# Performance work log

Measured on AMD Instinct MI355X. Metric: run time of the kernel, lower is better.

The kernel has to match this reference:

```python
import jax, jax.numpy as jnp
import numpy as np
from jax import lax

NB, C, HEADS, DH, MULT = 3, 64, 4, 16, 4  # num_blocks, dim, heads, dim_head, ffn mult

def _dw(x, k):
    # depthwise conv, NHWC, kernel HWIO with I=1, O=C, SAME padding
    return lax.conv_general_dilated(x, k, (1, 1), 'SAME',
                                    dimension_numbers=('NHWC', 'HWIO', 'NHWC'),
                                    feature_group_count=x.shape[-1])

def _l2n(t, eps=1e-6):
    # torch F.normalize(p=2, eps): x / max(||x||, eps) over last dim
    n = jnp.sqrt(jnp.sum(t * t, -1, keepdims=True))
    return t / jnp.maximum(n, eps)

def _ln(x, g, b, eps=1e-5):
    mu = jnp.mean(x, -1, keepdims=True)
    var = jnp.mean((x - mu) ** 2, -1, keepdims=True)
    return (x - mu) / jnp.sqrt(var + eps) * g + b

def _msa(x, m, Wq, Wk, Wv, resc, Wp, bp, pe1, pe2, w1, b1, w2, b2, dwk, db):
    # x, m: [b,h,w,c] (NHWC)
    b, h, w, c = x.shape
    n = h * w
    xf = x.reshape(b, n, c)
    q = xf @ Wq
    k = xf @ Wk
    v = xf @ Wv
    # mask-guided mechanism (1x1 convs == channel matmuls, 5x5 depthwise)
    m1 = m @ w1 + b1
    am = jax.nn.sigmoid(_dw(m1 @ w2 + b2, dwk) + db)
    ma = (m1 * am + m1).reshape(b, n, c)
    vg = v * ma  # mask gating of V (elementwise, head split commutes)
    hd = lambda t: t.reshape(b, n, HEADS, DH).transpose(0, 2, 3, 1)  # b,H,d,n
    qh = _l2n(hd(q))
    kh = _l2n(hd(k))
    vh = hd(vg)
    # transposed (channel) attention: [d,n]x[n,d] -> [d,d]
    attn = jnp.einsum('bhdn,bhen->bhde', kh, qh) * resc[None, :, None, None]
    attn = jax.nn.softmax(attn, -1)
    o = jnp.einsum('bhde,bhen->bhdn', attn, vh).transpose(0, 3, 1, 2).reshape(b, n, c)
    out_c = (o @ Wp + bp).reshape(b, h, w, c)
    # positional embedding on ungated v_inp: dwconv3 -> GELU -> dwconv3
    vi = v.reshape(b, h, w, c)
    out_p = _dw(jax.nn.gelu(_dw(vi, pe1), approximate=False), pe2)
    return out_c + out_p

def _ff(x, w1, dwk, w2):
    h1 = jax.nn.gelu(x @ w1, approximate=False)          # 1x1 conv expand
    h2 = jax.nn.gelu(_dw(h1, dwk), approximate=False)     # 3x3 depthwise
    return h2 @ w2                                        # 1x1 conv project

def setup_inputs() -> dict:
    key = jax.random.key(0)
    ks = iter(jax.random.split(key, 24))
    r = lambda sh, s=0.02: jax.random.normal(next(ks), sh, jnp.float32) * s
    B, H, W = 2, 256, 256
    return {
        'x': jax.random.normal(next(ks), (B, C, H, W), jnp.float32),
        'mask': jax.random.normal(next(ks), (B, C, H, W), jnp.float32),
        'Wq': r((NB, C, C)), 'Wk': r((NB, C, C)), 'Wv': r((NB, C, C)),
        'rescale': jnp.ones((NB, HEADS), jnp.float32),
        'Wp': r((NB, C, C)), 'bp': jnp.zeros((NB, C), jnp.float32),
        'pe1': r((NB, 3, 3, 1, C)), 'pe2': r((NB, 3, 3, 1, C)),
        'mm_w1': r((NB, C, C)), 'mm_b1': jnp.zeros((NB, C), jnp.float32),
        'mm_w2': r((NB, C, C)), 'mm_b2': jnp.zeros((NB, C), jnp.float32),
        'mm_dw': r((NB, 5, 5, 1, C)), 'mm_db': jnp.zeros((NB, C), jnp.float32),
        'ln_g': jnp.ones((NB, C), jnp.float32), 'ln_b': jnp.zeros((NB, C), jnp.float32),
        'ff_w1': r((NB, C, C * MULT)), 'ff_dw': r((NB, 3, 3, 1, C * MULT)),
        'ff_w2': r((NB, C * MULT, C)),
    }

def reference(x, mask, Wq, Wk, Wv, rescale, Wp, bp, pe1, pe2, mm_w1, mm_b1,
              mm_w2, mm_b2, mm_dw, mm_db, ln_g, ln_b, ff_w1, ff_dw, ff_w2):
    xh = x.transpose(0, 2, 3, 1)     # NCHW -> NHWC
    mh = mask.transpose(0, 2, 3, 1)
    for i in range(NB):
        xh = _msa(xh, mh, Wq[i], Wk[i], Wv[i], rescale[i], Wp[i], bp[i],
                  pe1[i], pe2[i], mm_w1[i], mm_b1[i], mm_w2[i], mm_b2[i],
                  mm_dw[i], mm_db[i]) + xh
        xh = _ff(_ln(xh, ln_g[i], ln_b[i]), ff_w1[i], ff_dw[i], ff_w2[i]) + xh
    return xh.transpose(0, 3, 1, 2)  # NHWC -> NCHW
```

## Files before the change

### kernel.cpp

```cpp
#include <hip/hip_runtime.h>
#include <math.h>


typedef unsigned short bhalf;
typedef unsigned int u32;
typedef _Float16 h2 __attribute__((ext_vector_type(2)));
typedef _Float16 f16x8 __attribute__((ext_vector_type(8)));
typedef __attribute__((ext_vector_type(4))) float f32x4;

#define GEMM_GRID 2048
#define NSPLIT 32
#define SCOPY 2304
#define WBLK 57344

__device__ __forceinline__ float h2f(bhalf b) {
  union { bhalf u; _Float16 h; } c; c.u = b; return (float)c.h;
}
__device__ __forceinline__ bhalf f2h(float f) {
  union { _Float16 h; bhalf u; } c; c.h = (_Float16)f; return c.u;
}
__device__ __forceinline__ u32 pack2h(float a, float b) {
  auto r = __builtin_amdgcn_cvt_pkrtz(a, b);
  union { decltype(r) h; u32 u; } c; c.h = r; return c.u;
}
__device__ __forceinline__ void unpack2h(u32 p, float& a, float& b) {
  union { u32 u; h2 h; } c; c.u = p;
  a = (float)c.h[0]; b = (float)c.h[1];
}
__device__ __forceinline__ void unpack8h(uint4 u, float* f) {
  unpack2h(u.x, f[0], f[1]); unpack2h(u.y, f[2], f[3]);
  unpack2h(u.z, f[4], f[5]); unpack2h(u.w, f[6], f[7]);
}
__device__ __forceinline__ float gelu_f(float v) {
  return 0.5f * v * (1.0f + erff(v * 0.70710678118654752440f));
}
__device__ __forceinline__ uint4 pack16(const float* v) {
  uint4 s;
  s.x = pack2h(v[0], v[1]); s.y = pack2h(v[2], v[3]);
  s.z = pack2h(v[4], v[5]); s.w = pack2h(v[6], v[7]);
  return s;
}

__global__ __launch_bounds__(256) void prep_weights(
    const float* __restrict__ mm_w1, const float* __restrict__ mm_w2,
    const float* __restrict__ Wq, const float* __restrict__ Wk,
    const float* __restrict__ Wv, const float* __restrict__ Wp,
    const float* __restrict__ ff_w1, const float* __restrict__ ff_w2,
    bhalf* __restrict__ out)
{
  int i = blockIdx.x >> 3, slot = blockIdx.x & 7;
  int t = threadIdx.x;
  const float* src; int ksh, N; size_t off;
  switch (slot) {
    case 0:  src = mm_w1 + i*4096;  ksh=6; N=64;  off = 0;     break;
    case 1:  src = mm_w2 + i*4096;  ksh=6; N=64;  off = 4096;  break;
    case 2:  src = Wq + i*4096;     ksh=6; N=64;  off = 8192;  break;
    case 3:  src = Wk + i*4096;     ksh=6; N=64;  off = 12288; break;
    case 4:  src = Wv + i*4096;     ksh=6; N=64;  off = 16384; break;
    case 5:  src = Wp + i*4096;     ksh=6; N=64;  off = 20480; break;
    case 6:  src = ff_w1 + i*16384; ksh=6; N=256; off = 24576; break;
    default: src = ff_w2 + i*16384; ksh=8; N=64;  off = 40960; break;
  }
  bhalf* dst = out + (size_t)i * WBLK + off;
  int sz = N << ksh;
  int kmask = (1 << ksh) - 1;
  for (int idx = t; idx < sz; idx += 256) {
    int n = idx >> ksh, k = idx & kmask;
    dst[idx] = f2h(src[k * N + n]);
  }
}

template<int MODE>
__global__ __launch_bounds__(256) void nchw2nhwc(const float* __restrict__ in,
                                                 void* __restrict__ out,
                                                 bhalf* __restrict__ out2) {
  __shared__ float tile[64][65];
  int t = threadIdx.x;
  int b = blockIdx.x >> 10;
  int n0 = (blockIdx.x & 1023) << 6;
  #pragma unroll
  for (int j = 0; j < 16; ++j) {
    int idx = j * 256 + t;
    int c = idx >> 6, nn = idx & 63;
    tile[c][nn] = in[(((size_t)(b * 64 + c)) << 16) + n0 + nn];
  }
  __syncthreads();
  #pragma unroll
  for (int j = 0; j < 16; ++j) {
    int idx = j * 256 + t;
    int nn = idx >> 6, c = idx & 63;
    size_t o = ((((size_t)b << 16) + n0 + nn) << 6) + c;
    float v = tile[c][nn];
    if (MODE == 0) { ((float*)out)[o] = v; out2[o] = f2h(v); }
    else           { ((bhalf*)out)[o] = f2h(v); }
  }
}

__global__ __launch_bounds__(256) void nhwc2nchw(const float* __restrict__ in,
                                                 float* __restrict__ out) {
  __shared__ float tile[64][65];
  int t = threadIdx.x;
  int b = blockIdx.x >> 10;
  int n0 = (blockIdx.x & 1023) << 6;
  #pragma unroll
  for (int j = 0; j < 16; ++j) {
    int idx = j * 256 + t;
    int nn = idx >> 6, c = idx & 63;
    tile[c][nn] = in[((((size_t)b << 16) + n0 + nn) << 6) + c];
  }
  __syncthreads();
  #pragma unroll
  for (int j = 0; j < 16; ++j) {
    int idx = j * 256 + t;
    int c = idx >> 6, nn = idx & 63;
    out[(((size_t)(b * 64 + c)) << 16) + n0 + nn] = tile[c][nn];
  }
}

__global__ __launch_bounds__(256) void gemm_mask2(
    const bhalf* __restrict__ M, const bhalf* __restrict__ wt,
    const float* __restrict__ b1, const float* __restrict__ b2,
    bhalf* __restrict__ T1o, bhalf* __restrict__ T2o)
{
  __shared__ __align__(16) char smem[9216 * 2 + 17408];
  bhalf* WT1 = (bhalf*)smem;
  bhalf* WT2 = (bhalf*)(smem + 9216);
  float* Cs  = (float*)(smem + 18432);
  bhalf* Ab  = (bhalf*)(smem + 18432);
  __shared__ float b1s[64], b2s[64];
  int t = threadIdx.x;
  {
    const uint4* ws = (const uint4*)wt;
    #pragma unroll
    for (int i = 0; i < 4; ++i) {
      int idx4 = i * 256 + t;
      int n = (idx4 >> 3) & 63, q4 = idx4 & 7;
      uint4* wd = (idx4 < 512) ? (uint4*)WT1 : (uint4*)WT2;
      wd[n * 9 + q4] = ws[idx4];
    }
    if (t < 64) { b1s[t] = b1[t]; b2s[t] = b2[t]; }
  }
  __syncthreads();

  int wv = t >> 6, lane = t & 63;
  int lm = lane & 15, q = lane >> 4;
  size_t row0 = ((size_t)blockIdx.x << 6) + (wv << 4);
  int rr = t >> 2, c0 = (t & 3) << 4;
  size_t grow = ((size_t)blockIdx.x << 6) + rr;

  const bhalf* arow = M + ((row0 + lm) << 6) + (q << 3);
  f16x8 a0 = *(const f16x8*)(arow);
  f16x8 a1 = *(const f16x8*)(arow + 32);
  f32x4 acc[4];
  #pragma unroll
  for (int nt = 0; nt < 4; ++nt) {
    const bhalf* bp_ = &WT1[(nt * 16 + lm) * 72 + (q << 3)];
    f16x8 bv0 = *(const f16x8*)(bp_);
    f16x8 bv1 = *(const f16x8*)(bp_ + 32);
    f32x4 c = {0.f, 0.f, 0.f, 0.f};
    c = __builtin_amdgcn_mfma_f32_16x16x32_f16(a0, bv0, c, 0, 0, 0);
    c = __builtin_amdgcn_mfma_f32_16x16x32_f16(a1, bv1, c, 0, 0, 0);
    acc[nt] = c;
  }
  #pragma unroll
  for (int nt = 0; nt < 4; ++nt)
    #pragma unroll
    for (int r = 0; r < 4; ++r)
      Cs[((wv << 4) + (q << 2) + r) * 68 + (nt << 4) + lm] = acc[nt][r];
  __syncthreads();
  float v[16];
  #pragma unroll
  for (int j = 0; j < 4; ++j) {
    float4 u = *(const float4*)&Cs[rr * 68 + c0 + 4 * j];
    v[4*j] = u.x; v[4*j+1] = u.y; v[4*j+2] = u.z; v[4*j+3] = u.w;
  }
  #pragma unroll
  for (int j = 0; j < 16; ++j) v[j] += b1s[c0 + j];
  uint4 p0 = pack16(v), p1 = pack16(v + 8);
  bhalf* ob1 = T1o + (grow << 6) + c0;
  ((uint4*)ob1)[0] = p0; ((uint4*)ob1)[1] = p1;
  __syncthreads();
  *(uint4*)&Ab[rr * 72 + c0]     = p0;
  *(uint4*)&Ab[rr * 72 + c0 + 8] = p1;
  __syncthreads();

  const bhalf* ar2 = &Ab[((wv << 4) + lm) * 72 + (q << 3)];
  f16x8 c0v = *(const f16x8*)(ar2);
  f16x8 c1v = *(const f16x8*)(ar2 + 32);
  #pragma unroll
  for (int nt = 0; nt < 4; ++nt) {
    const bhalf* bp_ = &WT2[(nt * 16 + lm) * 72 + (q << 3)];
    f16x8 bv0 = *(const f16x8*)(bp_);
    f16x8 bv1 = *(const f16x8*)(bp_ + 32);
    f32x4 c = {0.f, 0.f, 0.f, 0.f};
    c = __builtin_amdgcn_mfma_f32_16x16x32_f16(c0v, bv0, c, 0, 0, 0);
    c = __builtin_amdgcn_mfma_f32_16x16x32_f16(c1v, bv1, c, 0, 0, 0);
    acc[nt] = c;
  }
  __syncthreads();
  #pragma unroll
  for (int nt = 0; nt < 4; ++nt)
    #pragma unroll
    for (int r = 0; r < 4; ++r)
      Cs[((wv << 4) + (q << 2) + r) * 68 + (nt << 4) + lm] = acc[nt][r];
  __syncthreads();
  #pragma unroll
  for (int j = 0; j < 4; ++j) {
    float4 u = *(const float4*)&Cs[rr * 68 + c0 + 4 * j];
    v[4*j] = u.x; v[4*j+1] = u.y; v[4*j+2] = u.z; v[4*j+3] = u.w;
  }
  #pragma unroll
  for (int j = 0; j < 16; ++j) v[j] += b2s[c0 + j];
  bhalf* ob2 = T2o + (grow << 6) + c0;
  ((uint4*)ob2)[0] = pack16(v);
  ((uint4*)ob2)[1] = pack16(v + 8);
}

#define EP_BIAS 1
#define EP_RESID 5

template<int EP, int BW>
__global__ __launch_bounds__(256) void gemm64m(
    const bhalf* __restrict__ in_, const bhalf* __restrict__ wt,
    const float* __restrict__ bias, void* __restrict__ out_,
    const bhalf* __restrict__ aux, bhalf* __restrict__ xbout)
{
  __shared__ __align__(16) char smem[64 * 68 * 4];
  bhalf* WT = (bhalf*)smem;
  float* Cs = (float*)smem;
  __shared__ float bias_s[64];
  int t = threadIdx.x;
  if (BW) wt += (size_t)(blockIdx.x >> 10) << 12;
  {
    const uint4* ws = (const uint4*)wt;
    uint4* wd = (uint4*)WT;
    #pragma unroll
    for (int i = 0; i < 2; ++i) {
      int idx4 = i * 256 + t;
      int n = idx4 >> 3, q4 = idx4 & 7;
      wd[n * 9 + q4] = ws[idx4];
    }
    if (t < 64) bias_s[t] = bias[t];
  }
  __syncthreads();

  int wv = t >> 6, lane = t & 63;
  int lm = lane & 15, q = lane >> 4;
  size_t row0 = ((size_t)blockIdx.x << 6) + (wv << 4);

  const bhalf* arow = in_ + ((row0 + lm) << 6) + (q << 3);
  f16x8 a0 = *(const f16x8*)(arow);
  f16x8 a1 = *(const f16x8*)(arow + 32);

  f32x4 acc[4];
  #pragma unroll
  for (int nt = 0; nt < 4; ++nt) {
    const bhalf* bp_ = &WT[(nt * 16 + lm) * 72 + (q << 3)];
    f16x8 b0 = *(const f16x8*)(bp_);
    f16x8 b1 = *(const f16x8*)(bp_ + 32);
    f32x4 c = {0.f, 0.f, 0.f, 0.f};
    c = __builtin_amdgcn_mfma_f32_16x16x32_f16(a0, b0, c, 0, 0, 0);
    c = __builtin_amdgcn_mfma_f32_16x16x32_f16(a1, b1, c, 0, 0, 0);
    acc[nt] = c;
  }
  __syncthreads();
  #pragma unroll
  for (int nt = 0; nt < 4; ++nt)
    #pragma unroll
    for (int r = 0; r < 4; ++r)
      Cs[((wv << 4) + (q << 2) + r) * 68 + (nt << 4) + lm] = acc[nt][r];
  __syncthreads();

  int rr = t >> 2, c0 = (t & 3) << 4;
  size_t grow = ((size_t)blockIdx.x << 6) + rr;
  float v[16];
  #pragma unroll
  for (int j = 0; j < 4; ++j) {
    float4 u = *(const float4*)&Cs[rr * 68 + c0 + 4 * j];
    v[4*j] = u.x; v[4*j+1] = u.y; v[4*j+2] = u.z; v[4*j+3] = u.w;
  }

  if (EP == EP_RESID) {
    float* xr = (float*)out_ + (grow << 6) + c0;
    const bhalf* pr = aux + (grow << 6) + c0;
    uint4 p0 = ((const uint4*)pr)[0], p1 = ((const uint4*)pr)[1];
    float pf[16];
    unpack8h(p0, pf); unpack8h(p1, pf + 8);
    #pragma unroll
    for (int j = 0; j < 4; ++j) {
      float4* x4 = (float4*)(xr + 4 * j);
      float4 u = *x4;
      u.x += v[4*j]   + bias_s[c0 + 4*j]     + pf[4*j];
      u.y += v[4*j+1] + bias_s[c0 + 4*j + 1] + pf[4*j+1];
      u.z += v[4*j+2] + bias_s[c0 + 4*j + 2] + pf[4*j+2];
      u.w += v[4*j+3] + bias_s[c0 + 4*j + 3] + pf[4*j+3];
      *x4 = u;
      v[4*j] = u.x; v[4*j+1] = u.y; v[4*j+2] = u.z; v[4*j+3] = u.w;
    }
    bhalf* xb = xbout + (grow << 6) + c0;
    ((uint4*)xb)[0] = pack16(v);
    ((uint4*)xb)[1] = pack16(v + 8);
  } else {
    #pragma unroll
    for (int j = 0; j < 16; ++j) v[j] += bias_s[c0 + j];
    bhalf* ob = (bhalf*)out_ + (grow << 6) + c0;
    ((uint4*)ob)[0] = pack16(v);
    ((uint4*)ob)[1] = pack16(v + 8);
  }
}

__global__ __launch_bounds__(256) void qkv_gemm(
    const bhalf* __restrict__ xb, const bhalf* __restrict__ wt,
    const bhalf* __restrict__ ma, bhalf* __restrict__ Qb,
    bhalf* __restrict__ Kb, bhalf* __restrict__ Vb, bhalf* __restrict__ VG)
{
  __shared__ __align__(16) char smem[192 * 72 * 2];
  bhalf* WT = (bhalf*)smem;
  float* Cs = (float*)smem;
  int t = threadIdx.x;
  {
    const uint4* ws = (const uint4*)wt;
    uint4* wd = (uint4*)WT;
    #pragma unroll
    for (int i = 0; i < 6; ++i) {
      int idx4 = i * 256 + t;
      int n = idx4 >> 3, q4 = idx4 & 7;
      wd[n * 9 + q4] = ws[idx4];
    }
  }
  __syncthreads();

  int wv_ = t >> 6, lane = t & 63;
  int lm = lane & 15, q = lane >> 4;
  size_t row0 = ((size_t)blockIdx.x << 6) + (wv_ << 4);
  const bhalf* arow = xb + ((row0 + lm) << 6) + (q << 3);
  f16x8 a0 = *(const f16x8*)(arow);
  f16x8 a1 = *(const f16x8*)(arow + 32);

  f32x4 acc[12];
  #pragma unroll
  for (int nt = 0; nt < 12; ++nt) {
    const bhalf* bp_ = &WT[(nt * 16 + lm) * 72 + (q << 3)];
    f16x8 b0 = *(const f16x8*)(bp_);
    f16x8 b1 = *(const f16x8*)(bp_ + 32);
    f32x4 c = {0.f, 0.f, 0.f, 0.f};
    c = __builtin_amdgcn_mfma_f32_16x16x32_f16(a0, b0, c, 0, 0, 0);
    c = __builtin_amdgcn_mfma_f32_16x16x32_f16(a1, b1, c, 0, 0, 0);
    acc[nt] = c;
  }

  int rr = t >> 2, c0 = (t & 3) << 4;
  size_t grow = ((size_t)blockIdx.x << 6) + rr;
  #pragma unroll
  for (int g = 0; g < 3; ++g) {
    __syncthreads();
    #pragma unroll
    for (int nt = 0; nt < 4; ++nt)
      #pragma unroll
      for (int r = 0; r < 4; ++r)
        Cs[((wv_ << 4) + (q << 2) + r) * 68 + (nt << 4) + lm] = acc[g * 4 + nt][r];
    __syncthreads();
    float v[16];
    #pragma unroll
    for (int j = 0; j < 4; ++j) {
      float4 u = *(const float4*)&Cs[rr * 68 + c0 + 4 * j];
      v[4*j] = u.x; v[4*j+1] = u.y; v[4*j+2] = u.z; v[4*j+3] = u.w;
    }
    bhalf* ob = (g == 0 ? Qb : (g == 1 ? Kb : Vb)) + (grow << 6) + c0;
    ((uint4*)ob)[0] = pack16(v);
    ((uint4*)ob)[1] = pack16(v + 8);
    if (g == 2) {
      const bhalf* mr = ma + (grow << 6) + c0;
      uint4 m0 = ((const uint4*)mr)[0], m1q = ((const uint4*)mr)[1];
      float mf[16];
      unpack8h(m0, mf); unpack8h(m1q, mf + 8);
      float gv[16];
      #pragma unroll
      for (int j = 0; j < 16; ++j) gv[j] = v[j] * mf[j];
      bhalf* gb = VG + (grow << 6) + c0;
      ((uint4*)gb)[0] = pack16(gv);
      ((uint4*)gb)[1] = pack16(gv + 8);
    }
  }
}

__global__ __launch_bounds__(256) void ffn_gemm1_ln(
    const float* __restrict__ X, const bhalf* __restrict__ wt,
    const float* __restrict__ g, const float* __restrict__ bb,
    bhalf* __restrict__ out_)
{
  __shared__ __align__(16) char smem[256 * 72 * 2];
  bhalf* WT = (bhalf*)smem;
  float* Cs = (float*)smem;
  __shared__ float gs[64], bs[64];
  int t = threadIdx.x;
  {
    const uint4* ws = (const uint4*)wt;
    uint4* wd = (uint4*)WT;
    #pragma unroll
    for (int i = 0; i < 8; ++i) {
      int idx4 = i * 256 + t;
      int n = idx4 >> 3, q4 = idx4 & 7;
      wd[n * 9 + q4] = ws[idx4];
    }
    if (t < 64) { gs[t] = g[t]; bs[t] = bb[t]; }
  }
  __syncthreads();

  int wv_ = t >> 6, lane = t & 63;
  int lm = lane & 15, q = lane >> 4;
  size_t row0 = ((size_t)blockIdx.x << 6) + (wv_ << 4);
  const float* xr = X + ((row0 + lm) << 6);
  int k0 = q << 3;
  float xa[8], xb2[8];
  {
    float4 u0 = *(const float4*)(xr + k0);
    float4 u1 = *(const float4*)(xr + k0 + 4);
    float4 u2 = *(const float4*)(xr + 32 + k0);
    float4 u3 = *(const float4*)(xr + 32 + k0 + 4);
    xa[0]=u0.x; xa[1]=u0.y; xa[2]=u0.z; xa[3]=u0.w;
    xa[4]=u1.x; xa[5]=u1.y; xa[6]=u1.z; xa[7]=u1.w;
    xb2[0]=u2.x; xb2[1]=u2.y; xb2[2]=u2.z; xb2[3]=u2.w;
    xb2[4]=u3.x; xb2[5]=u3.y; xb2[6]=u3.z; xb2[7]=u3.w;
  }
  float s1 = 0.f, s2 = 0.f;
  #pragma unroll
  for (int j = 0; j < 8; ++j) {
    s1 += xa[j] + xb2[j];
    s2 += xa[j] * xa[j] + xb2[j] * xb2[j];
  }
  s1 += __shfl_xor(s1, 16); s1 += __shfl_xor(s1, 32);
  s2 += __shfl_xor(s2, 16); s2 += __shfl_xor(s2, 32);
  float mu = s1 * 0.015625f;
  float var = s2 * 0.015625f - mu * mu;
  float rstd = rsqrtf(var + 1e-5f);
  f16x8 a0, a1;
  #pragma unroll
  for (int j = 0; j < 8; ++j) {
    a0[j] = (_Float16)((xa[j]  - mu) * rstd * gs[k0 + j]      + bs[k0 + j]);
    a1[j] = (_Float16)((xb2[j] - mu) * rstd * gs[32 + k0 + j] + bs[32 + k0 + j]);
  }

  f32x4 acc[16];
  #pragma unroll
  for (int nt = 0; nt < 16; ++nt) {
    const bhalf* bp_ = &WT[(nt * 16 + lm) * 72 + (q << 3)];
    f16x8 b0 = *(const f16x8*)(bp_);
    f16x8 b1 = *(const f16x8*)(bp_ + 32);
    f32x4 c = {0.f, 0.f, 0.f, 0.f};
    c = __builtin_amdgcn_mfma_f32_16x16x32_f16(a0, b0, c, 0, 0, 0);
    c = __builtin_amdgcn_mfma_f32_16x16x32_f16(a1, b1, c, 0, 0, 0);
    acc[nt] = c;
  }

  int rr = t >> 2, c0 = (t & 3) << 4;
  size_t grow = ((size_t)blockIdx.x << 6) + rr;
  #pragma unroll
  for (int gi = 0; gi < 4; ++gi) {
    __syncthreads();
    #pragma unroll
    for (int nt = 0; nt < 4; ++nt)
      #pragma unroll
      for (int r = 0; r < 4; ++r)
        Cs[((wv_ << 4) + (q << 2) + r) * 68 + (nt << 4) + lm] = acc[gi * 4 + nt][r];
    __syncthreads();
    float v[16];
    #pragma unroll
    for (int j = 0; j < 4; ++j) {
      float4 u = *(const float4*)&Cs[rr * 68 + c0 + 4 * j];
      v[4*j]   = gelu_f(u.x); v[4*j+1] = gelu_f(u.y);
      v[4*j+2] = gelu_f(u.z); v[4*j+3] = gelu_f(u.w);
    }
    bhalf* ob = out_ + (grow << 8) + (gi << 6) + c0;
    ((uint4*)ob)[0] = pack16(v);
    ((uint4*)ob)[1] = pack16(v + 8);
  }
}

__global__ __launch_bounds__(256) void ffn_gemm2(
    const bhalf* __restrict__ in_, const bhalf* __restrict__ wt,
    float* __restrict__ X, bhalf* __restrict__ Xb)
{
  __shared__ __align__(16) char smem[64 * 264 * 2];
  bhalf* WT = (bhalf*)smem;
  float* Cs = (float*)smem;
  int t = threadIdx.x;
  {
    const uint4* ws = (const uint4*)wt;
    uint4* wd = (uint4*)WT;
    #pragma unroll
    for (int i = 0; i < 8; ++i) {
      int idx4 = i * 256 + t;
      int n = idx4 >> 5, q4 = idx4 & 31;
      wd[n * 33 + q4] = ws[idx4];
    }
  }
  __syncthreads();

  int wv_ = t >> 6, lane = t & 63;
  int lm = lane & 15, q = lane >> 4;
  size_t row0 = ((size_t)blockIdx.x << 6) + (wv_ << 4);
  const bhalf* arow = in_ + ((row0 + lm) << 8) + (q << 3);
  f16x8 a[8];
  #pragma unroll
  for (int ch = 0; ch < 8; ++ch) a[ch] = *(const f16x8*)(arow + 32 * ch);

  f32x4 acc[4];
  #pragma unroll
  for (int nt = 0; nt < 4; ++nt) {
    const bhalf* bp_ = &WT[(nt * 16 + lm) * 264 + (q << 3)];
    f32x4 c = {0.f, 0.f, 0.f, 0.f};
    #pragma unroll
    for (int ch = 0; ch < 8; ++ch) {
      f16x8 b = *(const f16x8*)(bp_ + 32 * ch);
      c = __builtin_amdgcn_mfma_f32_16x16x32_f16(a[ch], b, c, 0, 0, 0);
    }
    acc[nt] = c;
  }
  __syncthreads();
  #pragma unroll
  for (int nt = 0; nt < 4; ++nt)
    #pragma unroll
    for (int r = 0; r < 4; ++r)
      Cs[((wv_ << 4) + (q << 2) + r) * 68 + (nt << 4) + lm] = acc[nt][r];
  __syncthreads();

  int rr = t >> 2, c0 = (t & 3) << 4;
  size_t grow = ((size_t)blockIdx.x << 6) + rr;
  float v[16];
  #pragma unroll
  for (int j = 0; j < 4; ++j) {
    float4 u = *(const float4*)&Cs[rr * 68 + c0 + 4 * j];
    v[4*j] = u.x; v[4*j+1] = u.y; v[4*j+2] = u.z; v[4*j+3] = u.w;
  }
  float* xr = X + (grow << 6) + c0;
  #pragma unroll
  for (int j = 0; j < 4; ++j) {
    float4* x4 = (float4*)(xr + 4 * j);
    float4 u = *x4;
    u.x += v[4*j]; u.y += v[4*j+1]; u.z += v[4*j+2]; u.w += v[4*j+3];
    *x4 = u;
    v[4*j] = u.x; v[4*j+1] = u.y; v[4*j+2] = u.z; v[4*j+3] = u.w;
  }
  bhalf* xb = Xb + (grow << 6) + c0;
  ((uint4*)xb)[0] = pack16(v);
  ((uint4*)xb)[1] = pack16(v + 8);
}

template<int KS, int EPI, int CH>
__global__ __launch_bounds__(256) void dwconv4(
    const bhalf* __restrict__ in, const float* __restrict__ wt,
    const float* __restrict__ db, const bhalf* __restrict__ m1,
    bhalf* __restrict__ out, int wstride)
{
  const int CB = (CH == 64) ? 6 : 8;
  const int G  = CH >> 3;
  const int GB = (CH == 64) ? 3 : 5;
  const int R  = KS >> 1;
  const int NCOL = KS + 3;
  __shared__ u32 Wsu[KS * KS * G * 5];
  __shared__ float db_s[64];
  int t = threadIdx.x;
  for (int idx = t; idx < KS * KS * (CH >> 1); idx += 256) {
    int tap = idx >> (CB - 1), cp = idx & ((CH >> 1) - 1);
    int cg = cp >> 2, j = cp & 3;
    h2 p;
    p[0] = (_Float16)wt[tap * wstride + 2 * cp];
    p[1] = (_Float16)wt[tap * wstride + 2 * cp + 1];
    union { h2 h; u32 u; } cv; cv.h = p;
    Wsu[tap * (G * 5) + cg * 5 + j] = cv.u;
  }
  if (EPI == 2 && t < 64) db_s[t] = db[t];
  __syncthreads();

  size_t gid = (size_t)blockIdx.x * 256 + t;
  int cg = (int)gid & (G - 1);
  int c0 = cg << 3;
  size_t p4 = gid >> GB;
  int x0 = ((int)(p4 & 63)) << 2;
  int hy = (int)((p4 >> 6) & 255);
  size_t bb = p4 >> 14;

  h2 zero = {(_Float16)0.0f, (_Float16)0.0f};
  h2 acc[4][4];
  #pragma unroll
  for (int o = 0; o < 4; ++o)
    #pragma unroll
    for (int j = 0; j < 4; ++j) acc[o][j] = zero;

  #pragma unroll
  for (int kh = 0; kh < KS; ++kh) {
    int y = hy + kh - R;
    if ((unsigned)y >= 256u) continue;
    h2 wr[KS][4];
    #pragma unroll
    for (int kw = 0; kw < KS; ++kw) {
      const u32* wp = &Wsu[(kh * KS + kw) * (G * 5) + cg * 5];
      #pragma unroll
      for (int j = 0; j < 4; ++j) {
        union { u32 u; h2 h; } cv; cv.u = wp[j]; wr[kw][j] = cv.h;
      }
    }
    const bhalf* rowp = in + (((((size_t)bb << 8) + (size_t)y) << 8) << CB) + c0;
    #pragma unroll
    for (int cc = 0; cc < NCOL; ++cc) {
      int xw = x0 + cc - R;
      if (cc < R || cc >= NCOL - R) {
        if ((unsigned)xw >= 256u) continue;
      }
      union { uint4 u; h2 h[4]; } dv;
      dv.u = *(const uint4*)(rowp + ((size_t)xw << CB));
      #pragma unroll
      for (int kw = 0; kw < KS; ++kw) {
        int o = cc - kw;
        if (o >= 0 && o < 4) {
          #pragma unroll
          for (int j = 0; j < 4; ++j)
            acc[o][j] += dv.h[j] * wr[kw][j];
        }
      }
    }
  }

  size_t p0 = ((((size_t)bb << 8) + (size_t)hy) << 8) + (size_t)x0;
  #pragma unroll
  for (int o = 0; o < 4; ++o) {
    bhalf* op = out + ((p0 + o) << CB) + c0;
    if (EPI == 0) {
      union { h2 h[4]; uint4 u; } sv;
      #pragma unroll
      for (int j = 0; j < 4; ++j) sv.h[j] = acc[o][j];
      *(uint4*)op = sv.u;
    } else if (EPI == 1) {
      float r[8];
      #pragma unroll
      for (int j = 0; j < 4; ++j) {
        r[2*j]   = gelu_f((float)acc[o][j][0]);
        r[2*j+1] = gelu_f((float)acc[o][j][1]);
      }
      *(uint4*)op = pack16(r);
    } else {
      uint4 mu = *(const uint4*)(m1 + ((p0 + o) << CB) + c0);
      float mf[8];
      unpack8h(mu, mf);
      float r[8];
      #pragma unroll
      for (int j = 0; j < 8; ++j) {
        float av = (float)acc[o][j >> 1][j & 1];
        float am = 1.0f / (1.0f + expf(-(av + db_s[c0 + j])));
        r[j] = mf[j] * (am + 1.0f);
      }
      *(uint4*)op = pack16(r);
    }
  }
}

__global__ __launch_bounds__(256) void attn_partial2(
    const bhalf* __restrict__ Q, const bhalf* __restrict__ K,
    float* __restrict__ S)
{
  __shared__ bhalf Qs[64 * 64], Ks[64 * 64];
  int t = threadIdx.x;
  int h = t >> 6, lane = t & 63;
  int d = lane & 15, e4 = lane >> 4;
  int b = blockIdx.x >> 9;
  size_t rowbase = (size_t)blockIdx.x << 7;
  float acc[4] = {0.f, 0.f, 0.f, 0.f};
  float qss[4] = {0.f, 0.f, 0.f, 0.f};
  float kss = 0.f;
  for (int st = 0; st < 2; ++st) {
    __syncthreads();
    #pragma unroll
    for (int j = 0; j < 2; ++j) {
      int idx = j * 256 + t;
      int r = idx >> 3, seg = (idx & 7) << 3;
      size_t g = ((rowbase + (st << 6) + r) << 6) + seg;
      *(uint4*)&Qs[r * 64 + seg] = *(const uint4*)(Q + g);
      *(uint4*)&Ks[r * 64 + seg] = *(const uint4*)(K + g);
    }
    __syncthreads();
    #pragma unroll 8
    for (int r = 0; r < 64; ++r) {
      float kv = h2f(Ks[r * 64 + (h << 4) + d]);
      uint2 qu = *(const uint2*)&Qs[r * 64 + (h << 4) + (e4 << 2)];
      float q0, q1, q2, q3;
      unpack2h(qu.x, q0, q1); unpack2h(qu.y, q2, q3);
      acc[0] += kv * q0; acc[1] += kv * q1; acc[2] += kv * q2; acc[3] += kv * q3;
      qss[0] += q0 * q0; qss[1] += q1 * q1; qss[2] += q2 * q2; qss[3] += q3 * q3;
      kss += kv * kv;
    }
  }
  float* Sc = S + (size_t)(blockIdx.x & (NSPLIT - 1)) * SCOPY;
  float* Sp = Sc + ((((b * 4 + h) * 16 + d)) << 4) + (e4 << 2);
  atomicAdd(Sp + 0, acc[0]); atomicAdd(Sp + 1, acc[1]);
  atomicAdd(Sp + 2, acc[2]); atomicAdd(Sp + 3, acc[3]);
  if (d == 0) {
    float* qp = Sc + 2048 + b * 64 + (h << 4) + (e4 << 2);
    atomicAdd(qp + 0, qss[0]); atomicAdd(qp + 1, qss[1]);
    atomicAdd(qp + 2, qss[2]); atomicAdd(qp + 3, qss[3]);
  }
  if (e4 == 0) atomicAdd(Sc + 2176 + b * 64 + (h << 4) + d, kss);
}

__global__ void attn_softmax(const float* __restrict__ S,
                             const float* __restrict__ resc,
                             float* __restrict__ attnT)
{
  __shared__ float nqs[16];
  int b = blockIdx.x >> 2, h = blockIdx.x & 3;
  int d = threadIdx.x;
  float nqsum = 0.f, nksum = 0.f;
  for (int c = 0; c < NSPLIT; ++c) {
    nqsum += S[c * SCOPY + 2048 + b * 64 + h * 16 + d];
    nksum += S[c * SCOPY + 2176 + b * 64 + h * 16 + d];
  }
  nqs[d] = fmaxf(sqrtf(nqsum), 1e-6f);
  __syncthreads();
  float nkd = fmaxf(sqrtf(nksum), 1e-6f);
  float r = resc[h];
  float a[16];
  float4 s4[4] = {{0,0,0,0},{0,0,0,0},{0,0,0,0},{0,0,0,0}};
  for (int c = 0; c < NSPLIT; ++c) {
    const float4* sp = (const float4*)&S[c * SCOPY + (((b * 4 + h) * 16 + d) << 4)];
    #pragma unroll
    for (int j = 0; j < 4; ++j) {
      float4 u = sp[j];
      s4[j].x += u.x; s4[j].y += u.y; s4[j].z += u.z; s4[j].w += u.w;
    }
  }
  float m = -1e30f;
  #pragma unroll
  for (int j = 0; j < 4; ++j) {
    a[4*j]   = s4[j].x * r / (nkd * nqs[4*j]);
    a[4*j+1] = s4[j].y * r / (nkd * nqs[4*j+1]);
    a[4*j+2] = s4[j].z * r / (nkd * nqs[4*j+2]);
    a[4*j+3] = s4[j].w * r / (nkd * nqs[4*j+3]);
  }
  #pragma unroll
  for (int e = 0; e < 16; ++e) m = fmaxf(m, a[e]);
  float sum = 0.f;
  #pragma unroll
  for (int e = 0; e < 16; ++e) { a[e] = expf(a[e] - m); sum += a[e]; }
  float inv = 1.0f / sum;
  #pragma unroll
  for (int e = 0; e < 16; ++e)
    attnT[(((b * 4 + h) * 16 + e) << 4) + d] = a[e] * inv;
}

__global__ __launch_bounds__(256) void fold_attn(
    const float* __restrict__ attnT, const bhalf* __restrict__ wpT,
    bhalf* __restrict__ weffT)
{
  __shared__ float As[1024];
  int b = blockIdx.x;
  int t = threadIdx.x;
  #pragma unroll
  for (int j = 0; j < 4; ++j) As[j * 256 + t] = attnT[b * 1024 + j * 256 + t];
  __syncthreads();
  int m = t & 63, h = t >> 6;
  const bhalf* wp = wpT + m * 64 + h * 16;
  float wv_[16];
  uint4 w0 = ((const uint4*)wp)[0], w1 = ((const uint4*)wp)[1];
  unpack8h(w0, wv_); unpack8h(w1, wv_ + 8);
  float r[16];
  #pragma unroll
  for (int e = 0; e < 16; ++e) {
    const float* ar = &As[(h * 16 + e) << 4];
    float s = 0.f;
    #pragma unroll
    for (int d = 0; d < 16; ++d) s += ar[d] * wv_[d];
    r[e] = s;
  }
  bhalf* dst = weffT + b * 4096 + m * 64 + h * 16;
  ((uint4*)dst)[0] = pack16(r);
  ((uint4*)dst)[1] = pack16(r + 8);
}

extern "C" void kernel_launch(void* const* d_in, const int* in_sizes, int n_in,
                              void* d_out, int out_size, void* d_ws, size_t ws_size,
                              hipStream_t stream)
{
  (void)in_sizes; (void)n_in; (void)out_size; (void)ws_size;
  const float* x_in    = (const float*)d_in[0];
  const float* mask_in = (const float*)d_in[1];
  const float* Wq    = (const float*)d_in[2];
  const float* Wk    = (const float*)d_in[3];
  const float* Wv    = (const float*)d_in[4];
  const float* resc  = (const float*)d_in[5];
  const float* Wp    = (const float*)d_in[6];
  const float* bp    = (const float*)d_in[7];
  const float* pe1   = (const float*)d_in[8];
  const float* pe2   = (const float*)d_in[9];
  const float* mm_w1 = (const float*)d_in[10];
  const float* mm_b1 = (const float*)d_in[11];
  const float* mm_w2 = (const float*)d_in[12];
  const float* mm_b2 = (const float*)d_in[13];
  const float* mm_dw = (const float*)d_in[14];
  const float* mm_db = (const float*)d_in[15];
  const float* ln_g  = (const float*)d_in[16];
  const float* ln_b  = (const float*)d_in[17];
  const float* ff_w1 = (const float*)d_in[18];
  const float* ff_dw = (const float*)d_in[19];
  const float* ff_w2 = (const float*)d_in[20];

  const size_t NC = 8388608;
  char* w = (char*)d_ws;
  float* X  = (float*)w; w += NC * 4;
  bhalf* Xb = (bhalf*)w; w += NC * 2;
  bhalf* M  = (bhalf*)w; w += NC * 2;
  bhalf* Qb = (bhalf*)w; w += NC * 2;
  bhalf* Kb = (bhalf*)w; w += NC * 2;
  bhalf* Vb = (bhalf*)w; w += NC * 2;
  bhalf* VG = (bhalf*)w; w += NC * 2;
  bhalf* T1 = (bhalf*)w; w += NC * 2;
  bhalf* T2 = (bhalf*)w; w += NC * 2;
  bhalf* T3 = (bhalf*)w; w += NC * 2;
  bhalf* Pb = (bhalf*)w; w += NC * 2;
  float* Sb    = (float*)w; w += (size_t)NSPLIT * SCOPY * 4;
  float* attnT = (float*)w; w += 2048 * 4;
  bhalf* WeffT = (bhalf*)w; w += 8192 * 2;
  bhalf* WTg   = (bhalf*)w; w += (size_t)3 * WBLK * 2;
  bhalf* F1 = Qb;
  bhalf* F2 = T1;

  prep_weights<<<24, 256, 0, stream>>>(mm_w1, mm_w2, Wq, Wk, Wv, Wp, ff_w1, ff_w2, WTg);
  nchw2nhwc<0><<<2048, 256, 0, stream>>>(x_in, X, Xb);
  nchw2nhwc<1><<<2048, 256, 0, stream>>>(mask_in, M, nullptr);

  for (int i = 0; i < 3; ++i) {
    const bhalf* wb = WTg + (size_t)i * WBLK;
    gemm_mask2<<<GEMM_GRID, 256, 0, stream>>>(M, wb + 0, mm_b1 + i*64, mm_b2 + i*64, T1, T2);
    dwconv4<5, 2, 64><<<1024, 256, 0, stream>>>(T2, mm_dw + i*1600, mm_db + i*64, T1, T3, 64);
    qkv_gemm<<<GEMM_GRID, 256, 0, stream>>>(Xb, wb + 8192, T3, Qb, Kb, Vb, VG);
    hipMemsetAsync(Sb, 0, NSPLIT * SCOPY * 4, stream);
    attn_partial2<<<1024, 256, 0, stream>>>(Qb, Kb, Sb);
    attn_softmax<<<8, 16, 0, stream>>>(Sb, resc + i*4, attnT);
    fold_attn<<<2, 256, 0, stream>>>(attnT, wb + 20480, WeffT);
    dwconv4<3, 1, 64><<<1024, 256, 0, stream>>>(Vb, pe1 + i*576, nullptr, nullptr, T1, 64);
    dwconv4<3, 0, 64><<<1024, 256, 0, stream>>>(T1, pe2 + i*576, nullptr, nullptr, Pb, 64);
    gemm64m<EP_RESID, 1><<<GEMM_GRID, 256, 0, stream>>>(VG, WeffT, bp + i*64, X, Pb, Xb);
    ffn_gemm1_ln<<<GEMM_GRID, 256, 0, stream>>>(X, wb + 24576, ln_g + i*64, ln_b + i*64, F1);
    dwconv4<3, 1, 256><<<4096, 256, 0, stream>>>(F1, ff_dw + i*2304, nullptr, nullptr, F2, 256);
    ffn_gemm2<<<GEMM_GRID, 256, 0, stream>>>(F2, wb + 40960, X, Xb);
  }
  nhwc2nchw<<<2048, 256, 0, stream>>>(X, (float*)d_out);
}
```

Measured before the change: 918.4 us.

## Fuse K^T·Q partial reduction into QKV GEMM and merge softmax with Wp fold

The QKV GEMM epilogue now keeps the Q and K tiles in shared memory and computes the per-head K·Q^T partial sums and squared norms directly, accumulating them into the split buffers with atomics. This removes the Q/K global writes, the separate attn_partial2 kernel and its re-reads of Q and K. The softmax and projection fold are merged into a single attn_fold kernel, which also saves a launch and the attnT round trip. In exchange the GEMM kernel uses more shared memory and twice as many atomic blocks (2048 blocks each hitting the NSPLIT copies), which could raise atomic contention and lower occupancy.

After: 917.0 us. Within noise of the previous version (-0.2%).

```diff
diff --git a/kernel.cpp b/kernel.cpp
--- a/kernel.cpp
+++ b/kernel.cpp
@@ -311,12 +311,14 @@
 
 __global__ __launch_bounds__(256) void qkv_gemm(
     const bhalf* __restrict__ xb, const bhalf* __restrict__ wt,
-    const bhalf* __restrict__ ma, bhalf* __restrict__ Qb,
-    bhalf* __restrict__ Kb, bhalf* __restrict__ Vb, bhalf* __restrict__ VG)
+    const bhalf* __restrict__ ma, bhalf* __restrict__ Vb,
+    bhalf* __restrict__ VG, float* __restrict__ S)
 {
-  __shared__ __align__(16) char smem[192 * 72 * 2];
+  __shared__ __align__(16) char smem[35840];
   bhalf* WT = (bhalf*)smem;
   float* Cs = (float*)smem;
+  bhalf* Ks = (bhalf*)(smem + 17408);
+  bhalf* Qs = (bhalf*)(smem + 27648);
   int t = threadIdx.x;
   {
     const uint4* ws = (const uint4*)wt;
@@ -366,10 +368,17 @@
       float4 u = *(const float4*)&Cs[rr * 68 + c0 + 4 * j];
       v[4*j] = u.x; v[4*j+1] = u.y; v[4*j+2] = u.z; v[4*j+3] = u.w;
     }
-    bhalf* ob = (g == 0 ? Qb : (g == 1 ? Kb : Vb)) + (grow << 6) + c0;
-    ((uint4*)ob)[0] = pack16(v);
-    ((uint4*)ob)[1] = pack16(v + 8);
-    if (g == 2) {
+    uint4 o0 = pack16(v), o1 = pack16(v + 8);
+    if (g == 0) {
+      *(uint4*)&Qs[rr * 64 + c0] = o0;
+      *(uint4*)&Qs[rr * 64 + c0 + 8] = o1;
+    } else if (g == 1) {
+      *(uint4*)&Ks[rr * 64 + c0] = o0;
+      *(uint4*)&Ks[rr * 64 + c0 + 8] = o1;
+    } else {
+      bhalf* ob = Vb + (grow << 6) + c0;
+      ((uint4*)ob)[0] = o0;
+      ((uint4*)ob)[1] = o1;
       const bhalf* mr = ma + (grow << 6) + c0;
       uint4 m0 = ((const uint4*)mr)[0], m1q = ((const uint4*)mr)[1];
       float mf[16];
@@ -381,6 +390,34 @@
       ((uint4*)gb)[0] = pack16(gv);
       ((uint4*)gb)[1] = pack16(gv + 8);
     }
+  }
+
+  {
+    int d = lane & 15, e4 = lane >> 4;
+    int b = (int)(blockIdx.x >> 10);
+    float accS[4] = {0.f, 0.f, 0.f, 0.f};
+    float qss[4] = {0.f, 0.f, 0.f, 0.f};
+    float kss = 0.f;
+    #pragma unroll 8
+    for (int r = 0; r < 64; ++r) {
+      float kv = h2f(Ks[r * 64 + (wv_ << 4) + d]);
+      uint2 qu = *(const uint2*)&Qs[r * 64 + (wv_ << 4) + (e4 << 2)];
+      float q0, q1, q2, q3;
+      unpack2h(qu.x, q0, q1); unpack2h(qu.y, q2, q3);
+      accS[0] += kv * q0; accS[1] += kv * q1; accS[2] += kv * q2; accS[3] += kv * q3;
+      qss[0] += q0 * q0; qss[1] += q1 * q1; qss[2] += q2 * q2; qss[3] += q3 * q3;
+      kss += kv * kv;
+    }
+    float* Sc = S + (size_t)(blockIdx.x & (NSPLIT - 1)) * SCOPY;
+    float* Sp = Sc + (((b * 4 + wv_) * 16 + d) << 4) + (e4 << 2);
+    atomicAdd(Sp + 0, accS[0]); atomicAdd(Sp + 1, accS[1]);
+    atomicAdd(Sp + 2, accS[2]); atomicAdd(Sp + 3, accS[3]);
+    if (d == 0) {
+      float* qp = Sc + 2048 + b * 64 + (wv_ << 4) + (e4 << 2);
+      atomicAdd(qp + 0, qss[0]); atomicAdd(qp + 1, qss[1]);
+      atomicAdd(qp + 2, qss[2]); atomicAdd(qp + 3, qss[3]);
+    }
+    if (e4 == 0) atomicAdd(Sc + 2176 + b * 64 + (wv_ << 4) + d, kss);
   }
 }
 
@@ -655,125 +692,75 @@
   }
 }
 
-__global__ __launch_bounds__(256) void attn_partial2(
-    const bhalf* __restrict__ Q, const bhalf* __restrict__ K,
-    float* __restrict__ S)
-{
-  __shared__ bhalf Qs[64 * 64], Ks[64 * 64];
-  int t = threadIdx.x;
-  int h = t >> 6, lane = t & 63;
-  int d = lane & 15, e4 = lane >> 4;
-  int b = blockIdx.x >> 9;
-  size_t rowbase = (size_t)blockIdx.x << 7;
-  float acc[4] = {0.f, 0.f, 0.f, 0.f};
-  float qss[4] = {0.f, 0.f, 0.f, 0.f};
-  float kss = 0.f;
-  for (int st = 0; st < 2; ++st) {
-    __syncthreads();
-    #pragma unroll
-    for (int j = 0; j < 2; ++j) {
-      int idx = j * 256 + t;
-      int r = idx >> 3, seg = (idx & 7) << 3;
-      size_t g = ((rowbase + (st << 6) + r) << 6) + seg;
-      *(uint4*)&Qs[r * 64 + seg] = *(const uint4*)(Q + g);
-      *(uint4*)&Ks[r * 64 + seg] = *(const uint4*)(K + g);
-    }
-    __syncthreads();
-    #pragma unroll 8
-    for (int r = 0; r < 64; ++r) {
-      float kv = h2f(Ks[r * 64 + (h << 4) + d]);
-      uint2 qu = *(const uint2*)&Qs[r * 64 + (h << 4) + (e4 << 2)];
-      float q0, q1, q2, q3;
-      unpack2h(qu.x, q0, q1); unpack2h(qu.y, q2, q3);
-      acc[0] += kv * q0; acc[1] += kv * q1; acc[2] += kv * q2; acc[3] += kv * q3;
-      qss[0] += q0 * q0; qss[1] += q1 * q1; qss[2] += q2 * q2; qss[3] += q3 * q3;
-      kss += kv * kv;
-    }
-  }
-  float* Sc = S + (size_t)(blockIdx.x & (NSPLIT - 1)) * SCOPY;
-  float* Sp = Sc + ((((b * 4 + h) * 16 + d)) << 4) + (e4 << 2);
-  atomicAdd(Sp + 0, acc[0]); atomicAdd(Sp + 1, acc[1]);
-  atomicAdd(Sp + 2, acc[2]); atomicAdd(Sp + 3, acc[3]);
-  if (d == 0) {
-    float* qp = Sc + 2048 + b * 64 + (h << 4) + (e4 << 2);
-    atomicAdd(qp + 0, qss[0]); atomicAdd(qp + 1, qss[1]);
-    atomicAdd(qp + 2, qss[2]); atomicAdd(qp + 3, qss[3]);
-  }
-  if (e4 == 0) atomicAdd(Sc + 2176 + b * 64 + (h << 4) + d, kss);
-}
-
-__global__ void attn_softmax(const float* __restrict__ S,
-                             const float* __restrict__ resc,
-                             float* __restrict__ attnT)
-{
-  __shared__ float nqs[16];
-  int b = blockIdx.x >> 2, h = blockIdx.x & 3;
-  int d = threadIdx.x;
-  float nqsum = 0.f, nksum = 0.f;
-  for (int c = 0; c < NSPLIT; ++c) {
-    nqsum += S[c * SCOPY + 2048 + b * 64 + h * 16 + d];
-    nksum += S[c * SCOPY + 2176 + b * 64 + h * 16 + d];
-  }
-  nqs[d] = fmaxf(sqrtf(nqsum), 1e-6f);
-  __syncthreads();
-  float nkd = fmaxf(sqrtf(nksum), 1e-6f);
-  float r = resc[h];
-  float a[16];
-  float4 s4[4] = {{0,0,0,0},{0,0,0,0},{0,0,0,0},{0,0,0,0}};
-  for (int c = 0; c < NSPLIT; ++c) {
-    const float4* sp = (const float4*)&S[c * SCOPY + (((b * 4 + h) * 16 + d) << 4)];
-    #pragma unroll
-    for (int j = 0; j < 4; ++j) {
-      float4 u = sp[j];
-      s4[j].x += u.x; s4[j].y += u.y; s4[j].z += u.z; s4[j].w += u.w;
-    }
-  }
-  float m = -1e30f;
-  #pragma unroll
-  for (int j = 0; j < 4; ++j) {
-    a[4*j]   = s4[j].x * r / (nkd * nqs[4*j]);
-    a[4*j+1] = s4[j].y * r / (nkd * nqs[4*j+1]);
-    a[4*j+2] = s4[j].z * r / (nkd * nqs[4*j+2]);
-    a[4*j+3] = s4[j].w * r / (nkd * nqs[4*j+3]);
-  }
-  #pragma unroll
-  for (int e = 0; e < 16; ++e) m = fmaxf(m, a[e]);
-  float sum = 0.f;
-  #pragma unroll
-  for (int e = 0; e < 16; ++e) { a[e] = expf(a[e] - m); sum += a[e]; }
-  float inv = 1.0f / sum;
-  #pragma unroll
-  for (int e = 0; e < 16; ++e)
-    attnT[(((b * 4 + h) * 16 + e) << 4) + d] = a[e] * inv;
-}
-
-__global__ __launch_bounds__(256) void fold_attn(
-    const float* __restrict__ attnT, const bhalf* __restrict__ wpT,
-    bhalf* __restrict__ weffT)
+__global__ __launch_bounds__(256) void attn_fold(
+    const float* __restrict__ S, const float* __restrict__ resc,
+    const bhalf* __restrict__ wpT, bhalf* __restrict__ weffT)
 {
   __shared__ float As[1024];
+  __shared__ float nqs_s[64];
   int b = blockIdx.x;
   int t = threadIdx.x;
-  #pragma unroll
-  for (int j = 0; j < 4; ++j) As[j * 256 + t] = attnT[b * 1024 + j * 256 + t];
+  if (t < 64) {
+    int h = t >> 4, d = t & 15;
+    float nqsum = 0.f;
+    for (int c = 0; c < NSPLIT; ++c)
+      nqsum += S[c * SCOPY + 2048 + b * 64 + h * 16 + d];
+    nqs_s[t] = fmaxf(sqrtf(nqsum), 1e-6f);
+  }
+  __syncthreads();
+  if (t < 64) {
+    int h = t >> 4, d = t & 15;
+    float nksum = 0.f;
+    for (int c = 0; c < NSPLIT; ++c)
+      nksum += S[c * SCOPY + 2176 + b * 64 + h * 16 + d];
+    float nkd = fmaxf(sqrtf(nksum), 1e-6f);
+    float r = resc[h];
+    float4 s4[4] = {{0,0,0,0},{0,0,0,0},{0,0,0,0},{0,0,0,0}};
+    for (int c = 0; c < NSPLIT; ++c) {
+      const float4* sp = (const float4*)&S[c * SCOPY + (((b * 4 + h) * 16 + d) << 4)];
+      #pragma unroll
+      for (int j = 0; j < 4; ++j) {
+        float4 u = sp[j];
+        s4[j].x += u.x; s4[j].y += u.y; s4[j].z += u.z; s4[j].w += u.w;
+      }
+    }
+    float a[16];
+    #pragma unroll
+    for (int j = 0; j < 4; ++j) {
+      a[4*j]   = s4[j].x * r / (nkd * nqs_s[h * 16 + 4*j]);
+      a[4*j+1] = s4[j].y * r / (nkd * nqs_s[h * 16 + 4*j + 1]);
+      a[4*j+2] = s4[j].z * r / (nkd * nqs_s[h * 16 + 4*j + 2]);
+      a[4*j+3] = s4[j].w * r / (nkd * nqs_s[h * 16 + 4*j + 3]);
+    }
+    float m = -1e30f;
+    #pragma unroll
+    for (int e = 0; e < 16; ++e) m = fmaxf(m, a[e]);
+    float sum = 0.f;
+    #pragma unroll
+    for (int e = 0; e < 16; ++e) { a[e] = expf(a[e] - m); sum += a[e]; }
+    float inv = 1.0f / sum;
+    #pragma unroll
+    for (int e = 0; e < 16; ++e)
+      As[((h * 16 + e) << 4) + d] = a[e] * inv;
+  }
   __syncthreads();
   int m = t & 63, h = t >> 6;
   const bhalf* wp = wpT + m * 64 + h * 16;
   float wv_[16];
   uint4 w0 = ((const uint4*)wp)[0], w1 = ((const uint4*)wp)[1];
   unpack8h(w0, wv_); unpack8h(w1, wv_ + 8);
-  float r[16];
+  float r2[16];
   #pragma unroll
   for (int e = 0; e < 16; ++e) {
     const float* ar = &As[(h * 16 + e) << 4];
     float s = 0.f;
     #pragma unroll
     for (int d = 0; d < 16; ++d) s += ar[d] * wv_[d];
-    r[e] = s;
+    r2[e] = s;
   }
   bhalf* dst = weffT + b * 4096 + m * 64 + h * 16;
-  ((uint4*)dst)[0] = pack16(r);
-  ((uint4*)dst)[1] = pack16(r + 8);
+  ((uint4*)dst)[0] = pack16(r2);
+  ((uint4*)dst)[1] = pack16(r2 + 8);
 }
 
 extern "C" void kernel_launch(void* const* d_in, const int* in_sizes, int n_in,
@@ -817,9 +804,9 @@
   bhalf* T3 = (bhalf*)w; w += NC * 2;
   bhalf* Pb = (bhalf*)w; w += NC * 2;
   float* Sb    = (float*)w; w += (size_t)NSPLIT * SCOPY * 4;
-  float* attnT = (float*)w; w += 2048 * 4;
   bhalf* WeffT = (bhalf*)w; w += 8192 * 2;
   bhalf* WTg   = (bhalf*)w; w += (size_t)3 * WBLK * 2;
+  (void)Qb; (void)Kb;
   bhalf* F1 = Qb;
   bhalf* F2 = T1;
 
@@ -831,11 +818,9 @@
     const bhalf* wb = WTg + (size_t)i * WBLK;
     gemm_mask2<<<GEMM_GRID, 256, 0, stream>>>(M, wb + 0, mm_b1 + i*64, mm_b2 + i*64, T1, T2);
     dwconv4<5, 2, 64><<<1024, 256, 0, stream>>>(T2, mm_dw + i*1600, mm_db + i*64, T1, T3, 64);
-    qkv_gemm<<<GEMM_GRID, 256, 0, stream>>>(Xb, wb + 8192, T3, Qb, Kb, Vb, VG);
     hipMemsetAsync(Sb, 0, NSPLIT * SCOPY * 4, stream);
-    attn_partial2<<<1024, 256, 0, stream>>>(Qb, Kb, Sb);
-    attn_softmax<<<8, 16, 0, stream>>>(Sb, resc + i*4, attnT);
-    fold_attn<<<2, 256, 0, stream>>>(attnT, wb + 20480, WeffT);
+    qkv_gemm<<<GEMM_GRID, 256, 0, stream>>>(Xb, wb + 8192, T3, Vb, VG, Sb);
+    attn_fold<<<2, 256, 0, stream>>>(Sb, resc + i*4, wb + 20480, WeffT);
     dwconv4<3, 1, 64><<<1024, 256, 0, stream>>>(Vb, pe1 + i*576, nullptr, nullptr, T1, 64);
     dwconv4<3, 0, 64><<<1024, 256, 0, stream>>>(T1, pe2 + i*576, nullptr, nullptr, Pb, 64);
     gemm64m<EP_RESID, 1><<<GEMM_GRID, 256, 0, stream>>>(VG, WeffT, bp + i*64, X, Pb, Xb);
```
